# Performance work log

Hardware: AMD Instinct MI355X
Metric: run time of the kernel (lower is better)

The kernel has to match this reference:

```python
import jax, jax.numpy as jnp
import numpy as np

H = 128

def setup_inputs() -> dict:
    key = jax.random.key(0)
    ks = jax.random.split(key, 7)
    x = jax.random.normal(ks[0], (4, 65536, H), dtype=jnp.float32)
    # Linear(3H -> H) and Linear(H -> H), torch-style fan-in init scale
    W1 = jax.random.normal(ks[1], (3 * H, H), dtype=jnp.float32) / np.sqrt(3 * H)
    b1 = jax.random.normal(ks[2], (H,), dtype=jnp.float32) * 0.01
    W2 = jax.random.normal(ks[3], (H, H), dtype=jnp.float32) / np.sqrt(H)
    b2 = jax.random.normal(ks[4], (H,), dtype=jnp.float32) * 0.01
    gamma = jnp.ones((H,), dtype=jnp.float32)
    beta = jnp.zeros((H,), dtype=jnp.float32)
    return {"x": x, "W1": W1, "b1": b1, "W2": W2, "b2": b2, "gamma": gamma, "beta": beta}


def _layernorm(h, gamma, beta, eps=1e-5):
    mu = jnp.mean(h, axis=-1, keepdims=True)
    var = jnp.var(h, axis=-1, keepdims=True)
    return (h - mu) * jax.lax.rsqrt(var + eps) * gamma + beta


def reference(x, W1, b1, W2, b2, gamma, beta):
    # circular neighbor gather along node dim
    prev_x = jnp.roll(x, 1, axis=1)
    next_x = jnp.roll(x, -1, axis=1)
    cat = jnp.concatenate([prev_x, x, next_x], axis=-1)  # [B, N, 3H]
    h = jax.nn.relu(jnp.einsum('bnc,ch->bnh', cat, W1) + b1)
    delta = jnp.einsum('bnh,hk->bnk', h, W2) + b2
    return jax.nn.relu(_layernorm(x + delta, gamma, beta))
```

## Files before the change

kernel.cpp:

```cpp
#include <hip/hip_runtime.h>


typedef __bf16 bf16x8 __attribute__((ext_vector_type(8)));
typedef __bf16 bf16x4 __attribute__((ext_vector_type(4)));
typedef float  f32x4  __attribute__((ext_vector_type(4)));

#define H      128
#define NB     65536
#define TILE   64
#define XS     136
#define HSS    136
#define VS     132
#define NTILES 4096

__global__ __launch_bounds__(256, 2)
void cbb_kernel(const float* __restrict__ x, const float* __restrict__ W1,
                const float* __restrict__ b1, const float* __restrict__ W2,
                const float* __restrict__ b2, const float* __restrict__ gamma,
                const float* __restrict__ beta, float* __restrict__ out) {
    __shared__ __align__(16) char raw[(66 * XS + 64 * HSS) * 2];
    __bf16* xs = (__bf16*)raw;
    __bf16* hs = xs + 66 * XS;
    float*  vs = (float*)raw;
    __shared__ float s_mu[64], s_rs[64], s_gamma[128], s_beta[128];

    const int tid  = threadIdx.x;
    const int wid  = tid >> 6;
    const int lane = tid & 63;
    const int l    = lane & 15;
    const int g    = lane >> 4;
    const int col0 = wid * 32;
    const int c0   = col0 + l;
    const int c1   = col0 + 16 + l;

    if (tid < 128) { s_gamma[tid] = gamma[tid]; s_beta[tid] = beta[tid]; }

    const float b1r0 = b1[c0], b1r1 = b1[c1];
    const float b2r0 = b2[c0], b2r1 = b2[c1];

    bf16x8 w1f[12][2];
#pragma unroll
    for (int ks = 0; ks < 12; ++ks) {
#pragma unroll
        for (int ct = 0; ct < 2; ++ct) {
            const int cc = col0 + ct * 16 + l;
            bf16x8 f;
#pragma unroll
            for (int j = 0; j < 8; ++j)
                f[j] = (__bf16)W1[(ks * 32 + g * 8 + j) * H + cc];
            w1f[ks][ct] = f;
        }
    }
    bf16x8 w2f[4][2];
#pragma unroll
    for (int ks = 0; ks < 4; ++ks) {
#pragma unroll
        for (int ct = 0; ct < 2; ++ct) {
            const int cc = col0 + ct * 16 + l;
            bf16x8 f;
#pragma unroll
            for (int j = 0; j < 8; ++j)
                f[j] = (__bf16)W2[(ks * 32 + g * 8 + j) * H + cc];
            w2f[ks][ct] = f;
        }
    }

    for (int t = blockIdx.x; t < NTILES; t += gridDim.x) {
        const int b  = t >> 10;
        const int n0 = (t & 1023) << 6;
        const size_t rowbase = (size_t)b * NB;

        __syncthreads();

        for (int q = tid; q < 66 * 32; q += 256) {
            const int r = q >> 5, c = q & 31;
            const int grow = (n0 - 1 + r + NB) & (NB - 1);
            const float4 f = *(const float4*)(x + ((rowbase + grow) * H + c * 4));
            bf16x4 v4;
            v4[0] = (__bf16)f.x; v4[1] = (__bf16)f.y;
            v4[2] = (__bf16)f.z; v4[3] = (__bf16)f.w;
            *(bf16x4*)(xs + r * XS + c * 4) = v4;
        }
        __syncthreads();

        f32x4 acc[4][2];
#pragma unroll
        for (int rt = 0; rt < 4; ++rt)
#pragma unroll
            for (int ct = 0; ct < 2; ++ct)
                acc[rt][ct] = (f32x4){0.f, 0.f, 0.f, 0.f};

#pragma unroll
        for (int rt = 0; rt < 4; ++rt) {
            const int rb = rt * 16 + l;
#pragma unroll
            for (int ks = 0; ks < 12; ++ks) {
                const int k = ks * 32 + g * 8;
                const bf16x8 a = *(const bf16x8*)(xs + (rb + (k >> 7)) * XS + (k & 127));
                acc[rt][0] = __builtin_amdgcn_mfma_f32_16x16x32_bf16(a, w1f[ks][0], acc[rt][0], 0, 0, 0);
                acc[rt][1] = __builtin_amdgcn_mfma_f32_16x16x32_bf16(a, w1f[ks][1], acc[rt][1], 0, 0, 0);
            }
        }

#pragma unroll
        for (int rt = 0; rt < 4; ++rt) {
#pragma unroll
            for (int i = 0; i < 4; ++i) {
                const int row = rt * 16 + g * 4 + i;
                hs[row * HSS + c0] = (__bf16)fmaxf(acc[rt][0][i] + b1r0, 0.f);
                hs[row * HSS + c1] = (__bf16)fmaxf(acc[rt][1][i] + b1r1, 0.f);
            }
        }
        __syncthreads();

        f32x4 acc2[4][2];
#pragma unroll
        for (int rt = 0; rt < 4; ++rt)
#pragma unroll
            for (int ct = 0; ct < 2; ++ct)
                acc2[rt][ct] = (f32x4){0.f, 0.f, 0.f, 0.f};

#pragma unroll
        for (int rt = 0; rt < 4; ++rt) {
            const int rb = rt * 16 + l;
#pragma unroll
            for (int ks = 0; ks < 4; ++ks) {
                const bf16x8 a = *(const bf16x8*)(hs + rb * HSS + ks * 32 + g * 8);
                acc2[rt][0] = __builtin_amdgcn_mfma_f32_16x16x32_bf16(a, w2f[ks][0], acc2[rt][0], 0, 0, 0);
                acc2[rt][1] = __builtin_amdgcn_mfma_f32_16x16x32_bf16(a, w2f[ks][1], acc2[rt][1], 0, 0, 0);
            }
        }

#pragma unroll
        for (int rt = 0; rt < 4; ++rt) {
#pragma unroll
            for (int i = 0; i < 4; ++i) {
                const int row = rt * 16 + g * 4 + i;
                acc2[rt][0][i] += b2r0 + (float)xs[(row + 1) * XS + c0];
                acc2[rt][1][i] += b2r1 + (float)xs[(row + 1) * XS + c1];
            }
        }
        __syncthreads();

#pragma unroll
        for (int rt = 0; rt < 4; ++rt) {
#pragma unroll
            for (int i = 0; i < 4; ++i) {
                const int row = rt * 16 + g * 4 + i;
                vs[row * VS + c0] = acc2[rt][0][i];
                vs[row * VS + c1] = acc2[rt][1][i];
            }
        }
        __syncthreads();

        {
            const int row = tid >> 2;
            const int cb  = (tid & 3) * 32;
            float s = 0.f, qq = 0.f;
#pragma unroll
            for (int c8 = 0; c8 < 8; ++c8) {
                const f32x4 vv = *(const f32x4*)(vs + row * VS + cb + c8 * 4);
#pragma unroll
                for (int e = 0; e < 4; ++e) { s += vv[e]; qq += vv[e] * vv[e]; }
            }
            s  += __shfl_xor(s, 1, 4);  s  += __shfl_xor(s, 2, 4);
            qq += __shfl_xor(qq, 1, 4); qq += __shfl_xor(qq, 2, 4);
            const float muv = s * (1.f / 128.f);
            const float var = qq * (1.f / 128.f) - muv * muv;
            if ((tid & 3) == 0) { s_mu[row] = muv; s_rs[row] = rsqrtf(var + 1e-5f); }
        }
        __syncthreads();

        {
            const int row = tid >> 2;
            const int cb  = (tid & 3) * 32;
            const float muv = s_mu[row], rv = s_rs[row];
            float* op = out + (rowbase + n0 + row) * H + cb;
#pragma unroll
            for (int c8 = 0; c8 < 8; ++c8) {
                const f32x4 vv = *(const f32x4*)(vs + row * VS + cb + c8 * 4);
                const f32x4 gm = *(const f32x4*)(s_gamma + cb + c8 * 4);
                const f32x4 bt = *(const f32x4*)(s_beta + cb + c8 * 4);
                f32x4 o;
#pragma unroll
                for (int e = 0; e < 4; ++e)
                    o[e] = fmaxf((vv[e] - muv) * rv * gm[e] + bt[e], 0.f);
                *(f32x4*)(op + c8 * 4) = o;
            }
        }
    }
}

extern "C" void kernel_launch(void* const* d_in, const int* in_sizes, int n_in,
                              void* d_out, int out_size, void* d_ws, size_t ws_size,
                              hipStream_t stream) {
    const float* x     = (const float*)d_in[0];
    const float* W1    = (const float*)d_in[1];
    const float* b1    = (const float*)d_in[2];
    const float* W2    = (const float*)d_in[3];
    const float* b2    = (const float*)d_in[4];
    const float* gamma = (const float*)d_in[5];
    const float* beta  = (const float*)d_in[6];
    float* out = (float*)d_out;

    cbb_kernel<<<512, 256, 0, stream>>>(x, W1, b1, W2, b2, gamma, beta, out);
}
```

Before: 296.6 us.

## Stream pre-packed bf16 weights from global memory instead of holding them in registers

Adds a pre-pass kernel that converts W1 and W2 to bf16 and packs them into the per-lane MFMA fragment layout in workspace. The main kernel no longer keeps all weight fragments in registers. It instead loads each k-slice with vector loads, double-buffered one step ahead, and the loop order is swapped to ks-outer. The lower register use permits launch bounds of 4 blocks per CU and a 1024-block grid, aiming for more occupancy to hide memory latency. The cost is repeated L2/cache reads of the weights on every tile and an extra kernel launch.

```diff
diff --git a/kernel.cpp b/kernel.cpp
--- a/kernel.cpp
+++ b/kernel.cpp
@@ -13,11 +13,33 @@
 #define VS     132
 #define NTILES 4096
 
-__global__ __launch_bounds__(256, 2)
-void cbb_kernel(const float* __restrict__ x, const float* __restrict__ W1,
-                const float* __restrict__ b1, const float* __restrict__ W2,
+#define W1P_ELEMS 49152
+#define W2P_ELEMS 16384
+
+__global__ __launch_bounds__(256)
+void pack_w(const float* __restrict__ W1, const float* __restrict__ W2,
+            __bf16* __restrict__ wp) {
+    const int i = blockIdx.x * 256 + threadIdx.x;
+    if (i >= W1P_ELEMS + W2P_ELEMS) return;
+    const int isW2 = (i >= W1P_ELEMS);
+    const int ib = isW2 ? i - W1P_ELEMS : i;
+    const float* src = isW2 ? W2 : W1;
+    const int j    = ib & 7;
+    const int lane = (ib >> 3) & 63;
+    const int ct   = (ib >> 9) & 1;
+    const int w    = (ib >> 10) & 3;
+    const int ks   = ib >> 12;
+    const int row  = ks * 32 + (lane >> 4) * 8 + j;
+    const int col  = w * 32 + ct * 16 + (lane & 15);
+    wp[i] = (__bf16)src[row * H + col];
+}
+
+__global__ __launch_bounds__(256, 4)
+void cbb_kernel(const float* __restrict__ x,
+                const float* __restrict__ b1,
                 const float* __restrict__ b2, const float* __restrict__ gamma,
-                const float* __restrict__ beta, float* __restrict__ out) {
+                const float* __restrict__ beta,
+                const __bf16* __restrict__ wp, float* __restrict__ out) {
     __shared__ __align__(16) char raw[(66 * XS + 64 * HSS) * 2];
     __bf16* xs = (__bf16*)raw;
     __bf16* hs = xs + 66 * XS;
@@ -38,32 +60,8 @@
     const float b1r0 = b1[c0], b1r1 = b1[c1];
     const float b2r0 = b2[c0], b2r1 = b2[c1];
 
-    bf16x8 w1f[12][2];
-#pragma unroll
-    for (int ks = 0; ks < 12; ++ks) {
-#pragma unroll
-        for (int ct = 0; ct < 2; ++ct) {
-            const int cc = col0 + ct * 16 + l;
-            bf16x8 f;
-#pragma unroll
-            for (int j = 0; j < 8; ++j)
-                f[j] = (__bf16)W1[(ks * 32 + g * 8 + j) * H + cc];
-            w1f[ks][ct] = f;
-        }
-    }
-    bf16x8 w2f[4][2];
-#pragma unroll
-    for (int ks = 0; ks < 4; ++ks) {
-#pragma unroll
-        for (int ct = 0; ct < 2; ++ct) {
-            const int cc = col0 + ct * 16 + l;
-            bf16x8 f;
-#pragma unroll
-            for (int j = 0; j < 8; ++j)
-                f[j] = (__bf16)W2[(ks * 32 + g * 8 + j) * H + cc];
-            w2f[ks][ct] = f;
-        }
-    }
+    const __bf16* w1p = wp + (wid * 1024 + lane * 8);
+    const __bf16* w2p = wp + W1P_ELEMS + (wid * 1024 + lane * 8);
 
     for (int t = blockIdx.x; t < NTILES; t += gridDim.x) {
         const int b  = t >> 10;
@@ -90,16 +88,22 @@
             for (int ct = 0; ct < 2; ++ct)
                 acc[rt][ct] = (f32x4){0.f, 0.f, 0.f, 0.f};
 
-#pragma unroll
-        for (int rt = 0; rt < 4; ++rt) {
-            const int rb = rt * 16 + l;
-#pragma unroll
-            for (int ks = 0; ks < 12; ++ks) {
-                const int k = ks * 32 + g * 8;
+        bf16x8 wc0 = *(const bf16x8*)(w1p);
+        bf16x8 wc1 = *(const bf16x8*)(w1p + 512);
+#pragma unroll
+        for (int ks = 0; ks < 12; ++ks) {
+            const int ksn = (ks < 11) ? ks + 1 : 0;
+            bf16x8 wn0 = *(const bf16x8*)(w1p + ksn * 4096);
+            bf16x8 wn1 = *(const bf16x8*)(w1p + ksn * 4096 + 512);
+            const int k = ks * 32 + g * 8;
+#pragma unroll
+            for (int rt = 0; rt < 4; ++rt) {
+                const int rb = rt * 16 + l;
                 const bf16x8 a = *(const bf16x8*)(xs + (rb + (k >> 7)) * XS + (k & 127));
-                acc[rt][0] = __builtin_amdgcn_mfma_f32_16x16x32_bf16(a, w1f[ks][0], acc[rt][0], 0, 0, 0);
-                acc[rt][1] = __builtin_amdgcn_mfma_f32_16x16x32_bf16(a, w1f[ks][1], acc[rt][1], 0, 0, 0);
-            }
+                acc[rt][0] = __builtin_amdgcn_mfma_f32_16x16x32_bf16(a, wc0, acc[rt][0], 0, 0, 0);
+                acc[rt][1] = __builtin_amdgcn_mfma_f32_16x16x32_bf16(a, wc1, acc[rt][1], 0, 0, 0);
+            }
+            wc0 = wn0; wc1 = wn1;
         }
 
 #pragma unroll
@@ -120,15 +124,20 @@
             for (int ct = 0; ct < 2; ++ct)
                 acc2[rt][ct] = (f32x4){0.f, 0.f, 0.f, 0.f};
 
-#pragma unroll
-        for (int rt = 0; rt < 4; ++rt) {
-            const int rb = rt * 16 + l;
-#pragma unroll
-            for (int ks = 0; ks < 4; ++ks) {
-                const bf16x8 a = *(const bf16x8*)(hs + rb * HSS + ks * 32 + g * 8);
-                acc2[rt][0] = __builtin_amdgcn_mfma_f32_16x16x32_bf16(a, w2f[ks][0], acc2[rt][0], 0, 0, 0);
-                acc2[rt][1] = __builtin_amdgcn_mfma_f32_16x16x32_bf16(a, w2f[ks][1], acc2[rt][1], 0, 0, 0);
-            }
+        bf16x8 vc0 = *(const bf16x8*)(w2p);
+        bf16x8 vc1 = *(const bf16x8*)(w2p + 512);
+#pragma unroll
+        for (int ks = 0; ks < 4; ++ks) {
+            const int ksn = (ks < 3) ? ks + 1 : 0;
+            bf16x8 vn0 = *(const bf16x8*)(w2p + ksn * 4096);
+            bf16x8 vn1 = *(const bf16x8*)(w2p + ksn * 4096 + 512);
+#pragma unroll
+            for (int rt = 0; rt < 4; ++rt) {
+                const bf16x8 a = *(const bf16x8*)(hs + (rt * 16 + l) * HSS + ks * 32 + g * 8);
+                acc2[rt][0] = __builtin_amdgcn_mfma_f32_16x16x32_bf16(a, vc0, acc2[rt][0], 0, 0, 0);
+                acc2[rt][1] = __builtin_amdgcn_mfma_f32_16x16x32_bf16(a, vc1, acc2[rt][1], 0, 0, 0);
+            }
+            vc0 = vn0; vc1 = vn1;
         }
 
 #pragma unroll
@@ -202,6 +211,9 @@
     const float* gamma = (const float*)d_in[5];
     const float* beta  = (const float*)d_in[6];
     float* out = (float*)d_out;
-
-    cbb_kernel<<<512, 256, 0, stream>>>(x, W1, b1, W2, b2, gamma, beta, out);
+    __bf16* wp = (__bf16*)d_ws;
+
+    pack_w<<<256, 256, 0, stream>>>(W1, W2, wp);
+
+    cbb_kernel<<<1024, 256, 0, stream>>>(x, b1, b2, gamma, beta, wp, out);
 }
```

Measured after the change: 333.1 us. 1.12x slower.

## Prefetch next tile into registers and move W2 fragments to shared memory

Applied to the files above, without the earlier changes.

The next tile's x rows are loaded into registers right after the current tile is staged, so global loads overlap the MFMA work. Only the two halo rows are still fetched synchronously. W2 fragments now live in a 32KB shared buffer instead of registers, which frees VGPRs to hold the prefetch buffer. The cost is extra LDS reads per tile and higher LDS use per block, which could limit how many blocks fit per CU.

```diff
diff --git a/kernel.cpp b/kernel.cpp
--- a/kernel.cpp
+++ b/kernel.cpp
@@ -12,6 +12,7 @@
 #define HSS    136
 #define VS     132
 #define NTILES 4096
+#define GRID   512
 
 __global__ __launch_bounds__(256, 2)
 void cbb_kernel(const float* __restrict__ x, const float* __restrict__ W1,
@@ -22,6 +23,7 @@
     __bf16* xs = (__bf16*)raw;
     __bf16* hs = xs + 66 * XS;
     float*  vs = (float*)raw;
+    __shared__ __align__(16) __bf16 w2s[16384];
     __shared__ float s_mu[64], s_rs[64], s_gamma[128], s_beta[128];
 
     const int tid  = threadIdx.x;
@@ -51,28 +53,52 @@
             w1f[ks][ct] = f;
         }
     }
-    bf16x8 w2f[4][2];
-#pragma unroll
-    for (int ks = 0; ks < 4; ++ks) {
-#pragma unroll
-        for (int ct = 0; ct < 2; ++ct) {
-            const int cc = col0 + ct * 16 + l;
-            bf16x8 f;
-#pragma unroll
-            for (int j = 0; j < 8; ++j)
-                f[j] = (__bf16)W2[(ks * 32 + g * 8 + j) * H + cc];
-            w2f[ks][ct] = f;
-        }
-    }
-
-    for (int t = blockIdx.x; t < NTILES; t += gridDim.x) {
+
+    for (int idx = tid; idx < 16384; idx += 256) {
+        const int j  = idx & 7;
+        const int ln = (idx >> 3) & 63;
+        const int ct = (idx >> 9) & 1;
+        const int ks = (idx >> 10) & 3;
+        const int w  = idx >> 12;
+        const int row = ks * 32 + (ln >> 4) * 8 + j;
+        const int col = w * 32 + ct * 16 + (ln & 15);
+        w2s[idx] = (__bf16)W2[row * H + col];
+    }
+    const __bf16* w2w = w2s + wid * 4096;
+
+    float4 xreg[8];
+    {
+        const int t = blockIdx.x;
         const int b  = t >> 10;
         const int n0 = (t & 1023) << 6;
         const size_t rowbase = (size_t)b * NB;
-
-        __syncthreads();
-
-        for (int q = tid; q < 66 * 32; q += 256) {
+#pragma unroll
+        for (int s = 0; s < 8; ++s) {
+            const int q = tid + s * 256;
+            const int r = q >> 5, c = q & 31;
+            const int grow = (n0 - 1 + r + NB) & (NB - 1);
+            xreg[s] = *(const float4*)(x + ((rowbase + grow) * H + c * 4));
+        }
+    }
+
+    for (int t = blockIdx.x; t < NTILES; t += GRID) {
+        const int b  = t >> 10;
+        const int n0 = (t & 1023) << 6;
+        const size_t rowbase = (size_t)b * NB;
+
+        __syncthreads();
+
+#pragma unroll
+        for (int s = 0; s < 8; ++s) {
+            const int q = tid + s * 256;
+            const int r = q >> 5, c = q & 31;
+            bf16x4 v4;
+            v4[0] = (__bf16)xreg[s].x; v4[1] = (__bf16)xreg[s].y;
+            v4[2] = (__bf16)xreg[s].z; v4[3] = (__bf16)xreg[s].w;
+            *(bf16x4*)(xs + r * XS + c * 4) = v4;
+        }
+        if (tid < 64) {
+            const int q = 2048 + tid;
             const int r = q >> 5, c = q & 31;
             const int grow = (n0 - 1 + r + NB) & (NB - 1);
             const float4 f = *(const float4*)(x + ((rowbase + grow) * H + c * 4));
@@ -83,6 +109,20 @@
         }
         __syncthreads();
 
+        if (t + GRID < NTILES) {
+            const int tn  = t + GRID;
+            const int bn  = tn >> 10;
+            const int n0n = (tn & 1023) << 6;
+            const size_t rbn = (size_t)bn * NB;
+#pragma unroll
+            for (int s = 0; s < 8; ++s) {
+                const int q = tid + s * 256;
+                const int r = q >> 5, c = q & 31;
+                const int grow = (n0n - 1 + r + NB) & (NB - 1);
+                xreg[s] = *(const float4*)(x + ((rbn + grow) * H + c * 4));
+            }
+        }
+
         f32x4 acc[4][2];
 #pragma unroll
         for (int rt = 0; rt < 4; ++rt)
@@ -121,13 +161,14 @@
                 acc2[rt][ct] = (f32x4){0.f, 0.f, 0.f, 0.f};
 
 #pragma unroll
-        for (int rt = 0; rt < 4; ++rt) {
-            const int rb = rt * 16 + l;
-#pragma unroll
-            for (int ks = 0; ks < 4; ++ks) {
-                const bf16x8 a = *(const bf16x8*)(hs + rb * HSS + ks * 32 + g * 8);
-                acc2[rt][0] = __builtin_amdgcn_mfma_f32_16x16x32_bf16(a, w2f[ks][0], acc2[rt][0], 0, 0, 0);
-                acc2[rt][1] = __builtin_amdgcn_mfma_f32_16x16x32_bf16(a, w2f[ks][1], acc2[rt][1], 0, 0, 0);
+        for (int ks = 0; ks < 4; ++ks) {
+            const bf16x8 wf0 = *(const bf16x8*)(w2w + ks * 1024 + lane * 8);
+            const bf16x8 wf1 = *(const bf16x8*)(w2w + ks * 1024 + 512 + lane * 8);
+#pragma unroll
+            for (int rt = 0; rt < 4; ++rt) {
+                const bf16x8 a = *(const bf16x8*)(hs + (rt * 16 + l) * HSS + ks * 32 + g * 8);
+                acc2[rt][0] = __builtin_amdgcn_mfma_f32_16x16x32_bf16(a, wf0, acc2[rt][0], 0, 0, 0);
+                acc2[rt][1] = __builtin_amdgcn_mfma_f32_16x16x32_bf16(a, wf1, acc2[rt][1], 0, 0, 0);
             }
         }
 
@@ -203,5 +244,5 @@
     const float* beta  = (const float*)d_in[6];
     float* out = (float*)d_out;
 
-    cbb_kernel<<<512, 256, 0, stream>>>(x, W1, b1, W2, b2, gamma, beta, out);
+    cbb_kernel<<<GRID, 256, 0, stream>>>(x, W1, b1, W2, b2, gamma, beta, out);
 }
```

After: 270.3 us. 1.1x faster.
